# Performance work log

Measured on AMD Instinct MI355X. Metric: run time of the kernel, lower is better.

The kernel has to match this reference:

```python
import jax, jax.numpy as jnp
import numpy as np

DT = 1.0
S = 64            # num_sites
D = 2 * S         # state_dim
LOG_2PI = float(np.log(2.0 * np.pi))

def _selectors():
    s0 = np.zeros((2, 4), np.float32); s0[:, 0:2] = np.eye(2)
    s1 = np.zeros((2, 4), np.float32); s1[:, 2:4] = np.eye(2)
    cr = 0.5 * (s0 + s1)
    # [target=2, source=2, 2, 4]; off-diagonal pairs use the averaged selector
    return jnp.asarray(np.stack([np.stack([s0, cr]), np.stack([cr, s1])]))

SEL = _selectors()

def project_lon_lat(lon, lat):
    # lon, lat: [B,S]
    lat0 = lat.mean(-1, keepdims=True)
    lon0 = lon.mean(-1, keepdims=True)
    km = 111.32
    x = (lon - lon0) * (km * jnp.cos(jnp.deg2rad(lat0)))
    y = (lat - lat0) * km
    coords = jnp.stack([x, y], -1)                        # [B,S,2]
    h = coords[:, :, None, :] - coords[:, None, :, :]
    dist = jnp.sqrt((h ** 2).sum(-1) + 1e-12)
    npos = (dist > 1e-6).sum((-1, -2)).astype(coords.dtype)
    scale = dist.sum((-1, -2)) / jnp.maximum(npos, 1.0)
    return coords / jnp.maximum(scale, 1e-6)[:, None, None]

def build_A(h, mu, sigma, coupling, damping, eyeD):
    # h: [B,S,S,2], mu: [B,4], sigma: [B,4,4]
    B = mu.shape[0]
    sigma = 0.5 * (sigma + jnp.swapaxes(sigma, -1, -2))
    dm = jnp.einsum('tsab,nb->tsna', SEL, mu)                     # [2,2,B,2]
    dc = jnp.einsum('tsab,nbc,tsdc->tsnad', SEL, sigma, SEL)      # [2,2,B,2,2]
    dc = 0.5 * (dc + jnp.swapaxes(dc, -1, -2))
    eye2 = jnp.eye(2, dtype=h.dtype)
    Dm = (1.0 + 1e-4) * eye2 + (2.0 * DT ** 2) * dc
    Dinv = jnp.linalg.inv(Dm)
    _, logdet = jnp.linalg.slogdet(Dm)
    diff = h[None, None] - DT * dm[:, :, :, None, None, :]        # [2,2,B,S,S,2]
    q = jnp.einsum('tsbijd,tsbdf,tsbijf->tsbij', diff, Dinv, diff)
    ker = jnp.exp(-0.5 * (q + logdet[..., None, None]))
    ker = ker / jnp.maximum(ker.sum(-1, keepdims=True), 1e-6)
    ker = jnp.moveaxis(ker, 2, 0)                                 # [B,2,2,S,S]
    op = ker * coupling[None, :, :, None, None]
    op = jnp.transpose(op, (0, 1, 3, 2, 4)).reshape(B, D, D)
    return eyeD + DT * (op - damping * eyeD)

def _update(m, P, z_t, r2, eyeD):
    # Kalman measurement update with H = I, R = r2*I; returns per-sample NLL term
    Sm = P + r2 * eyeD
    v = z_t - m
    Sinv_v = jnp.linalg.solve(Sm, v[..., None])[..., 0]
    _, logdet = jnp.linalg.slogdet(Sm)
    nll_t = 0.5 * ((v * Sinv_v).sum(-1) + logdet + D * LOG_2PI)
    K = jnp.swapaxes(jnp.linalg.solve(Sm, P), -1, -2)   # P @ Sm^{-1} (P, Sm symmetric)
    m = m + jnp.einsum('bij,bj->bi', K, v)
    P = jnp.einsum('bij,bjk->bik', eyeD - K, P)
    return m, P, nll_t

def reference(z_seq, site_lon, site_lat, mu_seq, sigma_seq,
              log_q_proc, log_r_obs, log_p0, log_damping,
              init_mean, coupling_raw):
    B, T = z_seq.shape[0], z_seq.shape[1]
    z = z_seq.reshape(B, T, D)
    dtype = z.dtype
    eyeD = jnp.eye(D, dtype=dtype)
    r2 = jnp.exp(log_r_obs) ** 2
    q2 = jnp.exp(log_q_proc) ** 2
    damping = jnp.exp(log_damping)
    coupling = jnp.eye(2, dtype=dtype) + 0.25 * jnp.tanh(coupling_raw)

    lon = jnp.broadcast_to(site_lon[None], (B, S))
    lat = jnp.broadcast_to(site_lat[None], (B, S))
    coords = project_lon_lat(lon, lat)
    h = coords[:, :, None, :] - coords[:, None, :, :]   # [B,S,S,2]

    m0 = jnp.broadcast_to(init_mean[None], (B, D))
    P0 = jnp.broadcast_to(jnp.exp(log_p0) ** 2 * eyeD, (B, D, D))
    m, P, nll0 = _update(m0, P0, z[:, 0], r2, eyeD)

    def step(carry, xs):
        m, P = carry
        mu_t, sigma_t, z_t = xs
        A = build_A(h, mu_t, sigma_t, coupling, damping, eyeD)
        m = jnp.einsum('bij,bj->bi', A, m)
        P = jnp.einsum('bij,bjk,blk->bil', A, P, A) + q2 * eyeD
        m, P, nll_t = _update(m, P, z_t, r2, eyeD)
        return (m, P), nll_t

    xs = (jnp.swapaxes(mu_seq, 0, 1), jnp.swapaxes(sigma_seq, 0, 1),
          jnp.swapaxes(z[:, 1:], 0, 1))
    (_, _), nll_rest = jax.lax.scan(step, (m, P), xs)
    nll = nll0 + nll_rest.sum(0)   # [B]
    return nll.mean()

def setup_inputs() -> dict:
    key = jax.random.key(0)
    ks = jax.random.split(key, 5)
    B, T = 16, 128
    z_seq = jax.random.normal(ks[0], (B, T, S, 2), jnp.float32)
    site_lon = 10.0 + 0.5 * jax.random.uniform(ks[1], (S,), jnp.float32)
    site_lat = 55.0 + 0.5 * jax.random.uniform(ks[2], (S,), jnp.float32)
    mu_seq = 0.5 * jax.random.normal(ks[3], (B, T - 1, 4), jnp.float32)
    L = 0.2 * jax.random.normal(ks[4], (B, T - 1, 4, 4), jnp.float32)
    sigma_seq = jnp.einsum('btij,btkj->btik', L, L)   # PSD covariances
    return {
        'z_seq': z_seq, 'site_lon': site_lon, 'site_lat': site_lat,
        'mu_seq': mu_seq, 'sigma_seq': sigma_seq,
        'log_q_proc': jnp.float32(-2.0), 'log_r_obs': jnp.float32(-2.0),
        'log_p0': jnp.float32(0.0), 'log_damping': jnp.float32(0.0),
        'init_mean': jnp.zeros((D,), jnp.float32),
        'coupling_raw': jnp.zeros((2, 2), jnp.float32),
    }
```

## Files before the change

kernel.cpp:

```cpp
#include <hip/hip_runtime.h>
#include <math.h>


#define SQ 64
#define DQ 128
#define TQ 128
#define BQ 16
#define LDP 132
#define LDB 136
#define WFLOATS 17408
#define NTH 1024
#define LOG2PI 1.8378770664093454f

#define SMEM_FLOATS 35472

typedef __attribute__((ext_vector_type(8))) short bf16x8;
typedef __attribute__((ext_vector_type(4))) float f32x4;

__device__ __forceinline__ void lds_fence() {
  __asm__ volatile("s_waitcnt lgkmcnt(0)" ::: "memory");
}

__device__ __forceinline__ unsigned short f2bf(float f) {
  unsigned u = __float_as_uint(f);
  u += 0x7fffu + ((u >> 16) & 1u);
  return (unsigned short)(u >> 16);
}
__device__ __forceinline__ uint4 pack8(const float* v) {
  uint4 r;
  r.x = (unsigned)f2bf(v[0]) | ((unsigned)f2bf(v[1]) << 16);
  r.y = (unsigned)f2bf(v[2]) | ((unsigned)f2bf(v[3]) << 16);
  r.z = (unsigned)f2bf(v[4]) | ((unsigned)f2bf(v[5]) << 16);
  r.w = (unsigned)f2bf(v[6]) | ((unsigned)f2bf(v[7]) << 16);
  return r;
}

__device__ __forceinline__ float block_reduce_sum(float v, float* red) {
  #pragma unroll
  for (int off = 32; off > 0; off >>= 1) v += __shfl_down(v, off);
  const int tid = threadIdx.x;
  if ((tid & 63) == 0) red[tid >> 6] = v;
  __syncthreads();
  v = 0.0f;
  #pragma unroll
  for (int w = 0; w < NTH / 64; w++) v += red[w];
  __syncthreads();
  return v;
}

__device__ __forceinline__ void chol16_f(float* __restrict__ Wf,
                                         float* __restrict__ mdiag,
                                         int b0, int lane) {
  float a[16];
  if (lane < 16) {
    const float4* rp = (const float4*)(Wf + (b0 + lane) * LDP + b0);
    float4 q0 = rp[0], q1 = rp[1], q2v = rp[2], q3 = rp[3];
    a[0]=q0.x; a[1]=q0.y; a[2]=q0.z; a[3]=q0.w;
    a[4]=q1.x; a[5]=q1.y; a[6]=q1.z; a[7]=q1.w;
    a[8]=q2v.x; a[9]=q2v.y; a[10]=q2v.z; a[11]=q2v.w;
    a[12]=q3.x; a[13]=q3.y; a[14]=q3.z; a[15]=q3.w;
  } else {
    #pragma unroll
    for (int i = 0; i < 16; i++) a[i] = 1.0f;
  }
  float myrinv = 1.0f;
  #pragma unroll
  for (int j = 0; j < 16; j++) {
    float dj = __shfl(a[j], j);
    float rinv = rsqrtf(dj);
    float lij = a[j] * rinv;
    a[j] = lij;
    if (lane == j) myrinv = rinv;
    #pragma unroll
    for (int k = j + 1; k < 16; k++) {
      float lkj = __shfl(lij, k);
      a[k] = fmaf(-lij, lkj, a[k]);
    }
  }
  if (lane < 16) {
    float4* rp = (float4*)(Wf + (b0 + lane) * LDP + b0);
    rp[0] = make_float4(a[0], a[1], a[2], a[3]);
    rp[1] = make_float4(a[4], a[5], a[6], a[7]);
    rp[2] = make_float4(a[8], a[9], a[10], a[11]);
    rp[3] = make_float4(a[12], a[13], a[14], a[15]);
    mdiag[b0 + lane] = myrinv;
  }
}

__device__ __forceinline__ void trinv_chain2(float* __restrict__ Wf,
                                             const float* __restrict__ mdiag,
                                             int J, int pass, int lane) {
  const int c16 = lane & 15;
  const int j16 = 4 * (lane >> 4) + pass;
  const int sh = lane & 48;
  {
    float row[16];
    const float4* rp = (const float4*)(Wf + (J * 16 + c16) * LDP + J * 16);
    float4 a0 = rp[0], a1 = rp[1], a2 = rp[2], a3 = rp[3];
    row[0]=a0.x; row[1]=a0.y; row[2]=a0.z; row[3]=a0.w;
    row[4]=a1.x; row[5]=a1.y; row[6]=a1.z; row[7]=a1.w;
    row[8]=a2.x; row[9]=a2.y; row[10]=a2.z; row[11]=a2.w;
    row[12]=a3.x; row[13]=a3.y; row[14]=a3.z; row[15]=a3.w;
    float s = (c16 == j16) ? 1.0f : 0.0f;
    #pragma unroll
    for (int k = 0; k < 16; k++) {
      if (c16 == k) s *= mdiag[J * 16 + k];
      float sk = __shfl(s, sh | k);
      if (c16 > k) s = fmaf(-row[k], sk, s);
    }
    if (c16 > j16) Wf[(J * 16 + j16) * LDP + (J * 16 + c16)] = s;
  }
  lds_fence();
  const float md = mdiag[J * 16 + j16];
  const float* Mrow = Wf + (J * 16 + j16) * LDP + J * 16;
  #pragma unroll 1
  for (int I = J + 1; I < 8; I++) {
    const float* Lrow = Wf + (I * 16 + c16) * LDP + J * 16;
    float g = 0.0f;
    #pragma unroll
    for (int c4 = 0; c4 < 4; c4++) {
      float4 lv = *(const float4*)&Lrow[c4 * 4];
      float4 mq = *(const float4*)&Mrow[c4 * 4];
      float w0 = (c4*4+0 > j16) ? mq.x : ((c4*4+0 == j16) ? md : 0.0f);
      float w1 = (c4*4+1 > j16) ? mq.y : ((c4*4+1 == j16) ? md : 0.0f);
      float w2 = (c4*4+2 > j16) ? mq.z : ((c4*4+2 == j16) ? md : 0.0f);
      float w3 = (c4*4+3 > j16) ? mq.w : ((c4*4+3 == j16) ? md : 0.0f);
      g = fmaf(lv.x, w0, g); g = fmaf(lv.y, w1, g);
      g = fmaf(lv.z, w2, g); g = fmaf(lv.w, w3, g);
    }
    for (int K = J + 1; K < I; K++) {
      const float* LK = Lrow + (K - J) * 16;
      const float* MK = Wf + (J * 16 + j16) * LDP + K * 16;
      #pragma unroll
      for (int c4 = 0; c4 < 4; c4++) {
        float4 lv = *(const float4*)&LK[c4 * 4];
        float4 mq = *(const float4*)&MK[c4 * 4];
        g = fmaf(lv.x, mq.x, g); g = fmaf(lv.y, mq.y, g);
        g = fmaf(lv.z, mq.z, g); g = fmaf(lv.w, mq.w, g);
      }
    }
    float row2[16];
    {
      const float4* rp2 = (const float4*)(Wf + (I * 16 + c16) * LDP + I * 16);
      float4 a0 = rp2[0], a1 = rp2[1], a2 = rp2[2], a3 = rp2[3];
      row2[0]=a0.x; row2[1]=a0.y; row2[2]=a0.z; row2[3]=a0.w;
      row2[4]=a1.x; row2[5]=a1.y; row2[6]=a1.z; row2[7]=a1.w;
      row2[8]=a2.x; row2[9]=a2.y; row2[10]=a2.z; row2[11]=a2.w;
      row2[12]=a3.x; row2[13]=a3.y; row2[14]=a3.z; row2[15]=a3.w;
    }
    float sv = g;
    #pragma unroll
    for (int k = 0; k < 16; k++) {
      if (c16 == k) sv *= mdiag[I * 16 + k];
      float sk = __shfl(sv, sh | k);
      if (c16 > k) sv = fmaf(-row2[k], sk, sv);
    }
    Wf[(J * 16 + j16) * LDP + (I * 16 + c16)] = -sv;
    lds_fence();
  }
}

extern "C" __global__ __launch_bounds__(NTH, 4)
void ide_kf_kernel(const float* __restrict__ z_seq,
                   const float* __restrict__ site_lon,
                   const float* __restrict__ site_lat,
                   const float* __restrict__ mu_seq,
                   const float* __restrict__ sigma_seq,
                   const float* __restrict__ log_q,
                   const float* __restrict__ log_r,
                   const float* __restrict__ log_p0,
                   const float* __restrict__ log_damp,
                   const float* __restrict__ init_mean,
                   const float* __restrict__ coupling_raw,
                   float* __restrict__ ws) {
  extern __shared__ float smem[];
  float* Wf     = smem;
  float* B1f    = Wf + WFLOATS;
  float* B2f    = B1f + 8704;
  float* coords = B2f + 8704;
  float* mv     = coords + 128;
  float* vv     = mv + DQ;
  float* yv     = vv + DQ;
  float* mdiag  = yv + DQ;
  float* red    = mdiag + DQ;

  unsigned short* Tb  = (unsigned short*)Wf;
  unsigned short* Ab2 = (unsigned short*)Wf + 17408;
  unsigned short* Mtb = (unsigned short*)B1f;
  unsigned short* Pb  = (unsigned short*)B2f;

  const int tid = threadIdx.x;
  const int lane = tid & 63;
  const int wave = tid >> 6;
  const int rb = wave >> 1, ch = wave & 1;
  const int m16 = lane & 15, quad = lane >> 4;
  const int grp = wave >> 2, pass = wave & 3;
  const int b = blockIdx.x;
  float* nll_out = ws;

  const float r2 = __expf(2.0f * log_r[0]);
  const float q2 = __expf(2.0f * log_q[0]);
  const float p0sq = __expf(2.0f * log_p0[0]);
  const float damping = __expf(log_damp[0]);
  const float cpl00 = 1.0f + 0.25f * tanhf(coupling_raw[0]);
  const float cpl01 = 0.25f * tanhf(coupling_raw[1]);
  const float cpl10 = 0.25f * tanhf(coupling_raw[2]);
  const float cpl11 = 1.0f + 0.25f * tanhf(coupling_raw[3]);

  float myLon = (tid < SQ) ? site_lon[tid] : 0.0f;
  float myLat = (tid < SQ) ? site_lat[tid] : 0.0f;
  float lat0 = block_reduce_sum(myLat, red) * (1.0f / 64.0f);
  float lon0 = block_reduce_sum(myLon, red) * (1.0f / 64.0f);
  if (tid < SQ) {
    const float km = 111.32f;
    float cs = cosf(lat0 * 0.017453292519943295f);
    coords[2 * tid]     = (myLon - lon0) * (km * cs);
    coords[2 * tid + 1] = (myLat - lat0) * km;
  }
  __syncthreads();
  float dsum = 0.0f, dcnt = 0.0f;
  for (int idx = tid; idx < SQ * SQ; idx += NTH) {
    int i = idx >> 6, j = idx & 63;
    float dx = coords[2 * i] - coords[2 * j];
    float dy = coords[2 * i + 1] - coords[2 * j + 1];
    float d = sqrtf(dx * dx + dy * dy + 1e-12f);
    dsum += d;
    if (d > 1e-6f) dcnt += 1.0f;
  }
  dsum = block_reduce_sum(dsum, red);
  dcnt = block_reduce_sum(dcnt, red);
  float scale = dsum / fmaxf(dcnt, 1.0f);
  float sdiv = 1.0f / fmaxf(scale, 1e-6f);
  if (tid < SQ) { coords[2 * tid] *= sdiv; coords[2 * tid + 1] *= sdiv; }

  for (int e = tid; e < WFLOATS / 4; e += NTH)
    ((float4*)Wf)[e] = make_float4(0.0f, 0.0f, 0.0f, 0.0f);
  for (int e = tid; e < 8704 / 4; e += NTH)
    ((float4*)B2f)[e] = make_float4(0.0f, 0.0f, 0.0f, 0.0f);
  __syncthreads();
  if (tid < DQ) {
    Wf[tid * LDP + tid] = p0sq + r2;
    Pb[tid * LDB + tid] = f2bf(p0sq);
    mv[tid] = init_mean[tid];
  }
  __syncthreads();

  float nllp = 0.0f;

  #pragma unroll 1
  for (int t = 0; t < TQ; t++) {
    const float* zt = z_seq + ((size_t)b * TQ + t) * DQ;

    if (t > 0) {
      {
        f32x4 acc[4];
        #pragma unroll
        for (int c = 0; c < 4; c++) acc[c] = (f32x4){0.0f, 0.0f, 0.0f, 0.0f};
        #pragma unroll
        for (int ks = 0; ks < 4; ks++) {
          const int ko = 32 * ks + 8 * quad;
          bf16x8 a = *(const bf16x8*)(Ab2 + (16 * rb + m16) * LDB + ko);
          #pragma unroll
          for (int ct = 0; ct < 4; ct++) {
            bf16x8 bb = *(const bf16x8*)(Pb + (64 * ch + 16 * ct + m16) * LDB + ko);
            acc[ct] = __builtin_amdgcn_mfma_f32_16x16x32_bf16(a, bb, acc[ct], 0, 0, 0);
          }
        }
        #pragma unroll
        for (int ct = 0; ct < 4; ct++)
          #pragma unroll
          for (int reg = 0; reg < 4; reg++)
            Tb[(16 * rb + 4 * quad + reg) * LDB + 64 * ch + 16 * ct + m16] =
                f2bf(acc[ct][reg]);
        __syncthreads();
      }

      {
        const int ctmax = rb - 4 * ch;
        f32x4 acc[4];
        #pragma unroll
        for (int c = 0; c < 4; c++) acc[c] = (f32x4){0.0f, 0.0f, 0.0f, 0.0f};
        const bool gemv_wave = (wave == 1 || wave == 3);
        const int grow = (wave == 1) ? lane : 64 + lane;
        float newm = 0.0f;
        if (ctmax >= 0) {
          #pragma unroll
          for (int ks = 0; ks < 4; ks++) {
            const int ko = 32 * ks + 8 * quad;
            bf16x8 a = *(const bf16x8*)(Tb + (16 * rb + m16) * LDB + ko);
            #pragma unroll
            for (int ct = 0; ct < 4; ct++) {
              if (ct <= ctmax) {
                bf16x8 bb = *(const bf16x8*)(Ab2 + (64 * ch + 16 * ct + m16) * LDB + ko);
                acc[ct] = __builtin_amdgcn_mfma_f32_16x16x32_bf16(a, bb, acc[ct], 0, 0, 0);
              }
            }
          }
        } else if (gemv_wave) {
          const unsigned* ar = (const unsigned*)(Ab2 + grow * LDB);
          #pragma unroll 8
          for (int k2 = 0; k2 < 64; k2++) {
            unsigned p = ar[k2];
            newm = fmaf(__uint_as_float(p << 16), mv[2 * k2], newm);
            newm = fmaf(__uint_as_float(p & 0xffff0000u), mv[2 * k2 + 1], newm);
          }
        }
        __syncthreads();
        if (ctmax >= 0) {
          #pragma unroll
          for (int ct = 0; ct < 4; ct++) {
            if (ct <= ctmax) {
              #pragma unroll
              for (int reg = 0; reg < 4; reg++) {
                const int rg = 16 * rb + 4 * quad + reg;
                const int cgl = 64 * ch + 16 * ct + m16;
                Wf[rg * LDP + cgl] = acc[ct][reg] + ((rg == cgl) ? (q2 + r2) : 0.0f);
              }
            }
          }
        }
        if (gemv_wave) vv[grow] = zt[grow] - newm;
        if (wave == 0) {
          lds_fence();
          chol16_f(Wf, mdiag, 0, lane);
        }
        __syncthreads();
      }
    }

    if (t == 0) {
      if (tid < 64) {
        chol16_f(Wf, mdiag, 0, lane);
      } else if (tid < 192) {
        const int i = tid - 64;
        vv[i] = zt[i] - mv[i];
      }
      __syncthreads();
    }

    #pragma unroll 1
    for (int kb = 0; kb < 7; kb++) {
      const int b0k = kb * 16, base = b0k + 16, nbelow = DQ - base;
      if (tid < nbelow) {
        const int r = base + tid;
        float* wr = Wf + r * LDP + b0k;
        float w[16];
        #pragma unroll
        for (int u4 = 0; u4 < 4; u4++) {
          float4 w4 = *(const float4*)&wr[u4 * 4];
          w[u4*4] = w4.x; w[u4*4+1] = w4.y; w[u4*4+2] = w4.z; w[u4*4+3] = w4.w;
        }
        #pragma unroll
        for (int j = 0; j < 16; j++) {
          float s = w[j];
          #pragma unroll
          for (int l = 0; l < 16; l++) {
            if (l < j) s = fmaf(-w[l], Wf[(b0k + j) * LDP + b0k + l], s);
          }
          w[j] = s * mdiag[b0k + j];
        }
        #pragma unroll
        for (int u4 = 0; u4 < 4; u4++)
          *(float4*)&wr[u4 * 4] =
              make_float4(w[u4*4], w[u4*4+1], w[u4*4+2], w[u4*4+3]);
      }
      __syncthreads();
      if (tid < 64) {
        #pragma unroll
        for (int u = 0; u < 4; u++) {
          const int o = lane * 4 + u;
          const int mr = o >> 4, mc = o & 15;
          if (mr >= mc) {
            const float* pi = Wf + (base + mr) * LDP + b0k;
            const float* pj = Wf + (base + mc) * LDP + b0k;
            float s = 0.0f;
            #pragma unroll
            for (int c4 = 0; c4 < 4; c4++) {
              float4 xa = *(const float4*)&pi[c4 * 4];
              float4 yb = *(const float4*)&pj[c4 * 4];
              s = fmaf(xa.x, yb.x, s); s = fmaf(xa.y, yb.y, s);
              s = fmaf(xa.z, yb.z, s); s = fmaf(xa.w, yb.w, s);
            }
            Wf[(base + mr) * LDP + base + mc] -= s;
          }
        }
        chol16_f(Wf, mdiag, base, lane);
      } else if (tid >= 256) {
        const int grq = (tid >> 8) - 1;
        const int t8 = tid & 255;
        const int mrow = t8 >> 4, mcol = t8 & 15;
        const int mb = 7 - kb;
        int cnt = 0;
        for (int bi = 0; bi < mb; bi++) {
          for (int bj = 0; bj <= bi; bj++) {
            if (bi | bj) {
              if (cnt % 3 == grq && (bi > bj || mrow >= mcol)) {
                const int i = base + bi * 16 + mrow;
                const int j = base + bj * 16 + mcol;
                const float* pi = Wf + i * LDP + b0k;
                const float* pj = Wf + j * LDP + b0k;
                float s = 0.0f;
                #pragma unroll
                for (int c4 = 0; c4 < 4; c4++) {
                  float4 xa = *(const float4*)&pi[c4 * 4];
                  float4 yb = *(const float4*)&pj[c4 * 4];
                  s = fmaf(xa.x, yb.x, s); s = fmaf(xa.y, yb.y, s);
                  s = fmaf(xa.z, yb.z, s); s = fmaf(xa.w, yb.w, s);
                }
                Wf[i * LDP + j] -= s;
              }
              cnt++;
            }
          }
        }
      }
      __syncthreads();
    }

    {
      #pragma unroll 1
      for (int cc = 0; cc < 2; cc++) {
        const int J = cc ? (7 - grp) : grp;
        trinv_chain2(Wf, mdiag, J, pass, lane);
      }
      __syncthreads();
    }

    {
      const int mrow = tid >> 3, kc = (tid & 7) * 16;
      float mtv[16];
      if (kc > mrow) {
        const float4* rp = (const float4*)(Wf + mrow * LDP + kc);
        float4 q0 = rp[0], q1 = rp[1], q2v = rp[2], q3 = rp[3];
        mtv[0]=q0.x; mtv[1]=q0.y; mtv[2]=q0.z; mtv[3]=q0.w;
        mtv[4]=q1.x; mtv[5]=q1.y; mtv[6]=q1.z; mtv[7]=q1.w;
        mtv[8]=q2v.x; mtv[9]=q2v.y; mtv[10]=q2v.z; mtv[11]=q2v.w;
        mtv[12]=q3.x; mtv[13]=q3.y; mtv[14]=q3.z; mtv[15]=q3.w;
      } else if (kc + 15 < mrow) {
        #pragma unroll
        for (int u = 0; u < 16; u++) mtv[u] = 0.0f;
      } else {
        #pragma unroll
        for (int u = 0; u < 16; u++) {
          const int k = kc + u;
          mtv[u] = (k > mrow) ? Wf[mrow * LDP + k]
                 : ((k == mrow) ? mdiag[mrow] : 0.0f);
        }
      }
      if (tid < DQ) {
        nllp -= __logf(mdiag[tid]);
        float s = mdiag[tid] * vv[tid];
        for (int k = 0; k < tid; k++) s = fmaf(Wf[k * LDP + tid], vv[k], s);
        yv[tid] = s;
      }
      unsigned short* mt = Mtb + mrow * LDB + kc;
      *(uint4*)(mt) = pack8(mtv);
      *(uint4*)(mt + 8) = pack8(mtv + 8);
      __syncthreads();
    }

    {
      f32x4 acc[4];
      #pragma unroll
      for (int c = 0; c < 4; c++) acc[c] = (f32x4){0.0f, 0.0f, 0.0f, 0.0f};
      if (tid < DQ) nllp += 0.5f * yv[tid] * yv[tid];
      const int ctmax = rb - 4 * ch;
      if (ctmax >= 0) {
        for (int ks = (rb >> 1); ks < 4; ks++) {
          const int ko = 32 * ks + 8 * quad;
          bf16x8 a = *(const bf16x8*)(Mtb + (16 * rb + m16) * LDB + ko);
          #pragma unroll
          for (int ct = 0; ct < 4; ct++) {
            if (ct <= ctmax) {
              bf16x8 bb = *(const bf16x8*)(Mtb + (64 * ch + 16 * ct + m16) * LDB + ko);
              acc[ct] = __builtin_amdgcn_mfma_f32_16x16x32_bf16(a, bb, acc[ct], 0, 0, 0);
            }
          }
        }
      }
      const float nr22 = -r2 * r2;
      #pragma unroll
      for (int ct = 0; ct < 4; ct++) {
        if (ct <= ctmax) {
          const bool strict = (ct < ctmax);
          #pragma unroll
          for (int reg = 0; reg < 4; reg++) {
            const int rg = 16 * rb + 4 * quad + reg;
            const int cgl = 64 * ch + 16 * ct + m16;
            unsigned short hv = f2bf(nr22 * acc[ct][reg] + ((rg == cgl) ? r2 : 0.0f));
            Pb[rg * LDB + cgl] = hv;
            if (strict) Pb[cgl * LDB + rg] = hv;
          }
        }
      }
      if (tid < DQ) {
        const unsigned* mr = (const unsigned*)(Mtb + tid * LDB);
        float s = 0.0f;
        #pragma unroll 8
        for (int k2 = 0; k2 < 64; k2++) {
          unsigned p = mr[k2];
          s = fmaf(__uint_as_float(p << 16), yv[2 * k2], s);
          s = fmaf(__uint_as_float(p & 0xffff0000u), yv[2 * k2 + 1], s);
        }
        mv[tid] = zt[tid] - r2 * s;
      }
      if (t < TQ - 1) {
        const float* mu_t = mu_seq + ((size_t)b * (TQ - 1) + t) * 4;
        const float* sg_t = sigma_seq + ((size_t)b * (TQ - 1) + t) * 16;
        const int unit = tid >> 2, q = tid & 3;
        const int r = unit >> 1, ss = unit & 1, tt = r >> 6, i = r & 63;
        float m0 = mu_t[0], m1 = mu_t[1], m2 = mu_t[2], m3 = mu_t[3];
        float dmx, dmy, c00, c01, c11;
        if (tt == 0 && ss == 0) {
          dmx = m0; dmy = m1;
          c00 = sg_t[0]; c01 = 0.5f * (sg_t[1] + sg_t[4]); c11 = sg_t[5];
        } else if (tt == 1 && ss == 1) {
          dmx = m2; dmy = m3;
          c00 = sg_t[10]; c01 = 0.5f * (sg_t[11] + sg_t[14]); c11 = sg_t[15];
        } else {
          dmx = 0.5f * (m0 + m2); dmy = 0.5f * (m1 + m3);
          float s00 = sg_t[0];
          float s02 = 0.5f * (sg_t[2] + sg_t[8]);
          float s22 = sg_t[10];
          float s01 = 0.5f * (sg_t[1] + sg_t[4]);
          float s03 = 0.5f * (sg_t[3] + sg_t[12]);
          float s21 = 0.5f * (sg_t[9] + sg_t[6]);
          float s23 = 0.5f * (sg_t[11] + sg_t[14]);
          float s11 = sg_t[5];
          float s13 = 0.5f * (sg_t[7] + sg_t[13]);
          float s33 = sg_t[15];
          c00 = 0.25f * (s00 + s02 + s02 + s22);
          c01 = 0.25f * (s01 + s03 + s21 + s23);
          c11 = 0.25f * (s11 + s13 + s13 + s33);
        }
        float D00 = 1.0001f + 2.0f * c00;
        float D01 = 2.0f * c01;
        float D11 = 1.0001f + 2.0f * c11;
        float det = D00 * D11 - D01 * D01;
        float dinv = 1.0f / det;
        float d00 = D11 * dinv, d01 = -D01 * dinv, d11 = D00 * dinv;
        float ldts = __logf(det);
        float cix = coords[2 * i], ciy = coords[2 * i + 1];
        const float* cj = coords + q * 32;
        float kv[16];
        float rsum = 0.0f;
        #pragma unroll
        for (int u = 0; u < 16; u++) {
          float dx = cix - cj[2 * u] - dmx;
          float dy = ciy - cj[2 * u + 1] - dmy;
          float qf = d00 * dx * dx + 2.0f * d01 * dx * dy + d11 * dy * dy;
          kv[u] = __expf(-0.5f * (qf + ldts));
          rsum += kv[u];
        }
        float rtot = rsum + __shfl_xor(rsum, 1);
        rtot += __shfl_xor(rtot, 2);
        float cv = (tt == 0) ? ((ss == 0) ? cpl00 : cpl01)
                             : ((ss == 0) ? cpl10 : cpl11);
        float norm = cv / fmaxf(rtot, 1e-6f);
        #pragma unroll
        for (int u = 0; u < 16; u++) kv[u] *= norm;
        if (ss == tt && ((i >> 4) == q)) kv[i & 15] += 1.0f - damping;
        unsigned short* arow = Ab2 + r * LDB + ss * 64 + q * 16;
        *(uint4*)(arow) = pack8(kv);
        *(uint4*)(arow + 8) = pack8(kv + 8);
      }
      __syncthreads();
    }
  }

  float total = block_reduce_sum(nllp, red);
  if (tid == 0)
    nll_out[b] = total + (float)TQ * 0.5f * (float)DQ * LOG2PI;
}

extern "C" __global__ void ide_finalize(const float* __restrict__ part,
                                        float* __restrict__ out) {
  if (threadIdx.x == 0) {
    float s = 0.0f;
    for (int i = 0; i < BQ; i++) s += part[i];
    out[0] = s * (1.0f / BQ);
  }
}

extern "C" void kernel_launch(void* const* d_in, const int* in_sizes, int n_in,
                              void* d_out, int out_size, void* d_ws, size_t ws_size,
                              hipStream_t stream) {
  (void)in_sizes; (void)n_in; (void)out_size; (void)ws_size;
  const float* z_seq        = (const float*)d_in[0];
  const float* site_lon     = (const float*)d_in[1];
  const float* site_lat     = (const float*)d_in[2];
  const float* mu_seq       = (const float*)d_in[3];
  const float* sigma_seq    = (const float*)d_in[4];
  const float* log_q        = (const float*)d_in[5];
  const float* log_r        = (const float*)d_in[6];
  const float* log_p0       = (const float*)d_in[7];
  const float* log_damp     = (const float*)d_in[8];
  const float* init_mean    = (const float*)d_in[9];
  const float* coupling_raw = (const float*)d_in[10];
  float* ws = (float*)d_ws;
  float* out = (float*)d_out;

  const size_t smem_bytes = (size_t)SMEM_FLOATS * sizeof(float);
  hipFuncSetAttribute((const void*)ide_kf_kernel,
                      hipFuncAttributeMaxDynamicSharedMemorySize,
                      (int)smem_bytes);

  hipLaunchKernelGGL(ide_kf_kernel, dim3(BQ), dim3(NTH), smem_bytes, stream,
                     z_seq, site_lon, site_lat, mu_seq, sigma_seq,
                     log_q, log_r, log_p0, log_damp, init_mean, coupling_raw,
                     ws);
  hipLaunchKernelGGL(ide_finalize, dim3(1), dim3(64), 0, stream, ws, out);
}
```

Before: 9.437 ms.

## Use split-bf16 MFMA for Cholesky trailing updates instead of scalar FP32 dot products

Each solved 16-wide panel of the Cholesky factor is stored as bf16 hi/lo pairs. The update of the following diagonal block column is then computed with MFMA 16x16x32 bf16 instructions using a three-term split product, which stands in for the scalar FP32 dot-product loops. The work shifts from a lazy per-panel update of the whole trailing matrix to a left-looking update of only the next block column, one wave per 16-row block, with the diagonal block factored afterward. This aims to cut ALU time in the sequential Cholesky phase. It adds bf16 split precision error and reuses B1f/B2f as scratch, which requires those buffers to be free at that point.

```diff
diff --git a/kernel.cpp b/kernel.cpp
--- a/kernel.cpp
+++ b/kernel.cpp
@@ -188,6 +188,8 @@
   unsigned short* Ab2 = (unsigned short*)Wf + 17408;
   unsigned short* Mtb = (unsigned short*)B1f;
   unsigned short* Pb  = (unsigned short*)B2f;
+  unsigned short* Lhi = (unsigned short*)B1f;
+  unsigned short* Llo = (unsigned short*)B2f;
 
   const int tid = threadIdx.x;
   const int lane = tid & 63;
@@ -240,7 +242,6 @@
   __syncthreads();
   if (tid < DQ) {
     Wf[tid * LDP + tid] = p0sq + r2;
-    Pb[tid * LDB + tid] = f2bf(p0sq);
     mv[tid] = init_mean[tid];
   }
   __syncthreads();
@@ -363,55 +364,46 @@
         for (int u4 = 0; u4 < 4; u4++)
           *(float4*)&wr[u4 * 4] =
               make_float4(w[u4*4], w[u4*4+1], w[u4*4+2], w[u4*4+3]);
+        unsigned short hs[16]; float lo[16];
+        #pragma unroll
+        for (int u = 0; u < 16; u++) {
+          hs[u] = f2bf(w[u]);
+          lo[u] = w[u] - __uint_as_float(((unsigned)hs[u]) << 16);
+        }
+        uint4 h0, h1;
+        h0.x = hs[0] | ((unsigned)hs[1] << 16);   h0.y = hs[2] | ((unsigned)hs[3] << 16);
+        h0.z = hs[4] | ((unsigned)hs[5] << 16);   h0.w = hs[6] | ((unsigned)hs[7] << 16);
+        h1.x = hs[8] | ((unsigned)hs[9] << 16);   h1.y = hs[10] | ((unsigned)hs[11] << 16);
+        h1.z = hs[12] | ((unsigned)hs[13] << 16); h1.w = hs[14] | ((unsigned)hs[15] << 16);
+        unsigned short* hr = Lhi + r * LDB + b0k;
+        unsigned short* lr = Llo + r * LDB + b0k;
+        *(uint4*)(hr) = h0; *(uint4*)(hr + 8) = h1;
+        *(uint4*)(lr) = pack8(lo); *(uint4*)(lr + 8) = pack8(lo + 8);
+        const uint4 z4 = make_uint4(0u, 0u, 0u, 0u);
+        *(uint4*)(hr + 16) = z4; *(uint4*)(hr + 24) = z4;
+        *(uint4*)(lr + 16) = z4; *(uint4*)(lr + 24) = z4;
       }
       __syncthreads();
-      if (tid < 64) {
-        #pragma unroll
-        for (int u = 0; u < 4; u++) {
-          const int o = lane * 4 + u;
-          const int mr = o >> 4, mc = o & 15;
-          if (mr >= mc) {
-            const float* pi = Wf + (base + mr) * LDP + b0k;
-            const float* pj = Wf + (base + mc) * LDP + b0k;
-            float s = 0.0f;
-            #pragma unroll
-            for (int c4 = 0; c4 < 4; c4++) {
-              float4 xa = *(const float4*)&pi[c4 * 4];
-              float4 yb = *(const float4*)&pj[c4 * 4];
-              s = fmaf(xa.x, yb.x, s); s = fmaf(xa.y, yb.y, s);
-              s = fmaf(xa.z, yb.z, s); s = fmaf(xa.w, yb.w, s);
-            }
-            Wf[(base + mr) * LDP + base + mc] -= s;
-          }
-        }
-        chol16_f(Wf, mdiag, base, lane);
-      } else if (tid >= 256) {
-        const int grq = (tid >> 8) - 1;
-        const int t8 = tid & 255;
-        const int mrow = t8 >> 4, mcol = t8 & 15;
-        const int mb = 7 - kb;
-        int cnt = 0;
-        for (int bi = 0; bi < mb; bi++) {
-          for (int bj = 0; bj <= bi; bj++) {
-            if (bi | bj) {
-              if (cnt % 3 == grq && (bi > bj || mrow >= mcol)) {
-                const int i = base + bi * 16 + mrow;
-                const int j = base + bj * 16 + mcol;
-                const float* pi = Wf + i * LDP + b0k;
-                const float* pj = Wf + j * LDP + b0k;
-                float s = 0.0f;
-                #pragma unroll
-                for (int c4 = 0; c4 < 4; c4++) {
-                  float4 xa = *(const float4*)&pi[c4 * 4];
-                  float4 yb = *(const float4*)&pj[c4 * 4];
-                  s = fmaf(xa.x, yb.x, s); s = fmaf(xa.y, yb.y, s);
-                  s = fmaf(xa.z, yb.z, s); s = fmaf(xa.w, yb.w, s);
-                }
-                Wf[i * LDP + j] -= s;
-              }
-              cnt++;
-            }
-          }
+      if (wave <= 6 - kb) {
+        const int bi = kb + 1 + wave;
+        const int nch = (kb + 2) >> 1;
+        f32x4 acc = (f32x4){0.0f, 0.0f, 0.0f, 0.0f};
+        for (int c = 0; c < nch; c++) {
+          const int ko = 32 * c + 8 * quad;
+          bf16x8 ahi = *(const bf16x8*)(Lhi + (16 * bi + m16) * LDB + ko);
+          bf16x8 alo = *(const bf16x8*)(Llo + (16 * bi + m16) * LDB + ko);
+          bf16x8 bhi = *(const bf16x8*)(Lhi + (base + m16) * LDB + ko);
+          bf16x8 blo = *(const bf16x8*)(Llo + (base + m16) * LDB + ko);
+          acc = __builtin_amdgcn_mfma_f32_16x16x32_bf16(ahi, bhi, acc, 0, 0, 0);
+          acc = __builtin_amdgcn_mfma_f32_16x16x32_bf16(ahi, blo, acc, 0, 0, 0);
+          acc = __builtin_amdgcn_mfma_f32_16x16x32_bf16(alo, bhi, acc, 0, 0, 0);
+        }
+        #pragma unroll
+        for (int reg = 0; reg < 4; reg++)
+          Wf[(16 * bi + 4 * quad + reg) * LDP + base + m16] -= acc[reg];
+        if (wave == 0) {
+          lds_fence();
+          chol16_f(Wf, mdiag, base, lane);
         }
       }
       __syncthreads();
```

New measurement: 8.354 ms. 11.5% less time.
